# Performance work log

Measured on AMD Instinct MI355X. Metric: run time of the kernel, lower is better.

## Reference

```python
import jax, jax.numpy as jnp
import numpy as np

B, S, D = 4, 1024, 1280
H, DH = 20, 64          # n_head, d_hidden = embed_dim // n_head
DF = 4 * D              # r_ff = 4


def setup_inputs() -> dict:
    key = jax.random.key(0)
    ks = jax.random.split(key, 8)
    s_qkv = 1.0 / np.sqrt(D)
    inp = {
        "x": jax.random.normal(ks[0], (B, S, D), dtype=jnp.float32),
        # projection weights stored [in, out] so y = x @ W
        "Wq": jax.random.normal(ks[1], (D, H * DH), dtype=jnp.float32) * s_qkv,
        "Wk": jax.random.normal(ks[2], (D, H * DH), dtype=jnp.float32) * s_qkv,
        "Wv": jax.random.normal(ks[3], (D, H * DH), dtype=jnp.float32) * s_qkv,
        "ln_g": jnp.ones((D,), dtype=jnp.float32),
        "ln_b": jnp.zeros((D,), dtype=jnp.float32),
        "W1": jax.random.normal(ks[4], (D, DF), dtype=jnp.float32) * np.sqrt(2.0 / D),
        "b1": jnp.zeros((DF,), dtype=jnp.float32),
        "W2": jax.random.normal(ks[5], (DF, D), dtype=jnp.float32) * (1.0 / np.sqrt(DF)),
        "b2": jnp.zeros((D,), dtype=jnp.float32),
    }
    return inp


def reference(x, Wq, Wk, Wv, ln_g, ln_b, W1, b1, W2, b2):
    scaling = 1.0 / np.sqrt(DH)
    # --- Attention (note: original forward never applies to_out) ---
    q = (x @ Wq).reshape(B, S, H, DH) * scaling
    k = (x @ Wk).reshape(B, S, H, DH)
    v = (x @ Wv).reshape(B, S, H, DH)
    attn = jnp.einsum('bqhd,bkhd->bhqk', q, k)
    attn = jax.nn.softmax(attn, axis=-1)
    out = jnp.einsum('bhqk,bkhd->bqhd', attn, v).reshape(B, S, H * DH)
    x = out + x  # residual
    # --- FeedForward: LayerNorm -> linear1 -> relu -> linear2, residual ---
    mu = jnp.mean(x, axis=-1, keepdims=True)
    var = jnp.mean(jnp.square(x - mu), axis=-1, keepdims=True)
    h = (x - mu) * jax.lax.rsqrt(var + 1e-5) * ln_g + ln_b
    h = jax.nn.relu(h @ W1 + b1)
    h = h @ W2 + b2
    return x + h
```

## Files before the change

kernel.cpp:

```cpp
#include <hip/hip_runtime.h>
#include <hip/hip_bf16.h>

typedef short bf16x8 __attribute__((ext_vector_type(8)));
typedef float f32x4 __attribute__((ext_vector_type(4)));

typedef unsigned int u32_as1 __attribute__((address_space(1)));
typedef unsigned int u32_as3 __attribute__((address_space(3)));

#define B_ 4
#define S_ 1024
#define D_ 1280
#define H_ 20
#define DH_ 64
#define DF_ 5120
#define BS_ (B_*S_)
#define NQKV 3840

__device__ __forceinline__ void gld_lds16(const __hip_bfloat16* g, __hip_bfloat16* l) {
  __builtin_amdgcn_global_load_lds((const u32_as1*)g, (u32_as3*)l, 16, 0, 0);
}

__global__ __launch_bounds__(256) void cvt_f2b(
    const float* __restrict__ in, __hip_bfloat16* __restrict__ out, int n4)
{
  int i = blockIdx.x * 256 + threadIdx.x;
  if (i >= n4) return;
  const float4 v = ((const float4*)in)[i];
  __hip_bfloat16 o[4] = {__float2bfloat16(v.x), __float2bfloat16(v.y),
                         __float2bfloat16(v.z), __float2bfloat16(v.w)};
  *(short4*)(out + (size_t)i * 4) = *(short4*)o;
}

__global__ __launch_bounds__(256) void transpose_f2b(
    const float* __restrict__ in, __hip_bfloat16* __restrict__ out,
    int K, int N)
{
  __shared__ float tile[32][33];
  int k0 = blockIdx.x * 32, n0 = blockIdx.y * 32;
  int tx = threadIdx.x & 31, ty = threadIdx.x >> 5;
  #pragma unroll
  for (int i = 0; i < 32; i += 8)
    tile[ty + i][tx] = in[(size_t)(k0 + ty + i) * N + n0 + tx];
  __syncthreads();
  #pragma unroll
  for (int i = 0; i < 32; i += 8)
    out[(size_t)(n0 + ty + i) * K + k0 + tx] = __float2bfloat16(tile[tx][ty + i]);
}

__global__ __launch_bounds__(256) void transpose_v(
    const __hip_bfloat16* __restrict__ qkv, __hip_bfloat16* __restrict__ vT)
{
  __shared__ __hip_bfloat16 tile[32][33];
  int s0 = blockIdx.x * 32;
  int d0 = blockIdx.y * 32;
  int bh = blockIdx.z;
  int b = bh / H_, h = bh - b * H_;
  int tx = threadIdx.x & 31, ty = threadIdx.x >> 5;
  const __hip_bfloat16* src = qkv + (size_t)b * S_ * NQKV + 2 * D_ + h * DH_;
  #pragma unroll
  for (int i = 0; i < 32; i += 8)
    tile[ty + i][tx] = src[(size_t)(s0 + ty + i) * NQKV + d0 + tx];
  __syncthreads();
  __hip_bfloat16* dst = vT + (size_t)bh * DH_ * S_;
  #pragma unroll
  for (int i = 0; i < 32; i += 8)
    dst[(size_t)(d0 + ty + i) * S_ + s0 + tx] = tile[tx][ty + i];
}

template<int EPI>
__global__ __launch_bounds__(512, 2) void gemm256(
    const __hip_bfloat16* __restrict__ A,
    const __hip_bfloat16* __restrict__ BT,
    const float* __restrict__ bias,
    __hip_bfloat16* __restrict__ C,
    float* __restrict__ Cf0,
    float* __restrict__ Cf1,
    int M, int N, int K, int Kext)
{
  __shared__ __align__(16) __hip_bfloat16 As[2][2][256 * 32];
  __shared__ __align__(16) __hip_bfloat16 Bs[2][2][256 * 32];
  __hip_bfloat16* AsF = &As[0][0][0];
  __hip_bfloat16* BsF = &Bs[0][0][0];

  const int t = threadIdx.x;
  const int lane = t & 63;
  const int wave = t >> 6;
  const int wm = wave >> 2, wn = wave & 3;
  const int quad = lane >> 4, l16 = lane & 15;
  const int bm = blockIdx.x * 256, bn = blockIdx.y * 256;
  const int koff = blockIdx.z * Kext;
  const int Kc = (K - koff < Kext) ? (K - koff) : Kext;
  const int NT = Kc >> 6;

  const int srow = t >> 2;
  const int sc = (t & 3) ^ ((t >> 3) & 3);
  const __hip_bfloat16* Ag = A  + (size_t)(bm + srow) * K + koff + sc * 8;
  const __hip_bfloat16* Bg = BT + (size_t)(bn + srow) * K + koff + sc * 8;
  const size_t rq = (size_t)128 * K;

  const int swz = quad ^ ((l16 >> 1) & 3);
  const int aob = (wm * 128 + l16) * 32 + swz * 8;
  const int bob = (wn * 64 + l16) * 32 + swz * 8;

  f32x4 acc[8][4];
  #pragma unroll
  for (int i = 0; i < 8; i++)
    #pragma unroll
    for (int j = 0; j < 4; j++)
      acc[i][j] = (f32x4){0.f, 0.f, 0.f, 0.f};

#define STAGE_A(u_, kk_, b_) do { \
    const __hip_bfloat16* g_ = Ag + (size_t)(u_) * 64 + (kk_) * 32; \
    gld_lds16(g_,      AsF + ((b_) * 2 + (kk_)) * 8192 + t * 8); \
    gld_lds16(g_ + rq, AsF + ((b_) * 2 + (kk_)) * 8192 + 4096 + t * 8); \
  } while (0)
#define STAGE_B(u_, kk_, b_) do { \
    const __hip_bfloat16* g_ = Bg + (size_t)(u_) * 64 + (kk_) * 32; \
    gld_lds16(g_,      BsF + ((b_) * 2 + (kk_)) * 8192 + t * 8); \
    gld_lds16(g_ + rq, BsF + ((b_) * 2 + (kk_)) * 8192 + 4096 + t * 8); \
  } while (0)

  STAGE_A(0, 0, 0); STAGE_B(0, 0, 0); STAGE_A(0, 1, 0); STAGE_B(0, 1, 0);
  STAGE_B(1, 0, 1); STAGE_A(1, 0, 1); STAGE_B(1, 1, 1);
  asm volatile("s_waitcnt vmcnt(6)" ::: "memory");
  __builtin_amdgcn_s_barrier();
  asm volatile("" ::: "memory");

  bf16x8 av[4], bv[4];

#define PHASE_MFMA(ibase_) \
    __builtin_amdgcn_s_barrier(); \
    asm volatile("s_waitcnt lgkmcnt(0)" ::: "memory"); \
    __builtin_amdgcn_s_setprio(1); \
    _Pragma("unroll") \
    for (int i = 0; i < 4; i++) \
      _Pragma("unroll") \
      for (int j = 0; j < 4; j++) \
        acc[(ibase_) + i][j] = __builtin_amdgcn_mfma_f32_16x16x32_bf16(av[i], bv[j], acc[(ibase_) + i][j], 0, 0, 0); \
    __builtin_amdgcn_s_setprio(0); \
    __builtin_amdgcn_s_barrier(); \
    asm volatile("" ::: "memory");

#define TILE_BODY(u_, B_) do { \
    const int hb0 = (B_) * 2 * 8192, hb1 = ((B_) * 2 + 1) * 8192; \
     \
    _Pragma("unroll") \
    for (int i = 0; i < 4; i++) av[i] = *(const bf16x8*)(AsF + hb0 + aob + i * 512); \
    _Pragma("unroll") \
    for (int j = 0; j < 4; j++) bv[j] = *(const bf16x8*)(BsF + hb0 + bob + j * 512); \
    if ((u_) + 1 < NT) STAGE_A((u_) + 1, 1, (B_) ^ 1); \
    PHASE_MFMA(0) \
     \
    _Pragma("unroll") \
    for (int i = 0; i < 4; i++) av[i] = *(const bf16x8*)(AsF + hb0 + aob + (i + 4) * 512); \
    if ((u_) + 2 < NT) STAGE_B((u_) + 2, 0, (B_)); \
    PHASE_MFMA(4) \
     \
    _Pragma("unroll") \
    for (int i = 0; i < 4; i++) av[i] = *(const bf16x8*)(AsF + hb1 + aob + i * 512); \
    _Pragma("unroll") \
    for (int j = 0; j < 4; j++) bv[j] = *(const bf16x8*)(BsF + hb1 + bob + j * 512); \
    if ((u_) + 2 < NT) STAGE_A((u_) + 2, 0, (B_)); \
    PHASE_MFMA(0) \
     \
    _Pragma("unroll") \
    for (int i = 0; i < 4; i++) av[i] = *(const bf16x8*)(AsF + hb1 + aob + (i + 4) * 512); \
    if ((u_) + 2 < NT) { \
      STAGE_B((u_) + 2, 1, (B_)); \
      asm volatile("s_waitcnt vmcnt(6)" ::: "memory"); \
    } else { \
      asm volatile("s_waitcnt vmcnt(0)" ::: "memory"); \
    } \
    PHASE_MFMA(4) \
  } while (0)

  for (int u = 0; u < NT; u += 2) {
    TILE_BODY(u, 0);
    TILE_BODY(u + 1, 1);
  }

#undef TILE_BODY
#undef PHASE_MFMA
#undef STAGE_A
#undef STAGE_B

  float* Cf = (blockIdx.z == 0) ? Cf0 : Cf1;
  #pragma unroll
  for (int i = 0; i < 8; i++) {
    #pragma unroll
    for (int j = 0; j < 4; j++) {
      int col = bn + wn * 64 + j * 16 + l16;
      #pragma unroll
      for (int r = 0; r < 4; r++) {
        int row = bm + wm * 128 + i * 16 + quad * 4 + r;
        float v = acc[i][j][r];
        if (EPI == 1) { v += bias[col]; v = fmaxf(v, 0.f); }
        if (EPI == 3) {
          Cf[(size_t)row * N + col] = v;
        } else {
          C[(size_t)row * N + col] = __float2bfloat16(v);
        }
      }
    }
  }
}

__global__ __launch_bounds__(256) void ffn2_reduce(
    const float* __restrict__ P0, const float* __restrict__ P1,
    const float* __restrict__ bias, const float* __restrict__ resid,
    float* __restrict__ out)
{
  int i = blockIdx.x * 256 + threadIdx.x;
  float4 p0 = ((const float4*)P0)[i];
  float4 p1 = ((const float4*)P1)[i];
  float4 r  = ((const float4*)resid)[i];
  float4 b  = ((const float4*)bias)[i % (D_ / 4)];
  float4 o;
  o.x = p0.x + p1.x + r.x + b.x;
  o.y = p0.y + p1.y + r.y + b.y;
  o.z = p0.z + p1.z + r.z + b.z;
  o.w = p0.w + p1.w + r.w + b.w;
  ((float4*)out)[i] = o;
}

__global__ __launch_bounds__(256) void attn_mfma(
    const __hip_bfloat16* __restrict__ qkv,
    const __hip_bfloat16* __restrict__ vT,
    const float* __restrict__ x,
    float* __restrict__ x1)
{
  const int qt = blockIdx.x, h = blockIdx.y, b = blockIdx.z;
  const int t = threadIdx.x;
  const int lane = t & 63;
  const int wave = t >> 6;
  const int quad = lane >> 4, l16 = lane & 15;

  __shared__ __hip_bfloat16 Ks[2][64 * 64];
  __shared__ __hip_bfloat16 Vs[2][64 * 64];
  __shared__ short Pl[4][16][72];

  const int qrow0 = qt * 128 + wave * 32;
  const size_t tok0 = (size_t)b * S_;
  const int qcol = h * DH_;
  const int kcol = D_ + h * DH_;
  const size_t vtbase = (size_t)(b * H_ + h) * DH_ * S_;

  const int s1i = t + 256;
  const int r0 = t >> 3,   c0 = (t & 7)   ^ (r0 & 7);
  const int r1 = s1i >> 3, c1 = (s1i & 7) ^ (r1 & 7);
  const __hip_bfloat16* Kg0 = qkv + (tok0 + r0) * NQKV + kcol + c0 * 8;
  const __hip_bfloat16* Kg1 = qkv + (tok0 + r1) * NQKV + kcol + c1 * 8;
  const __hip_bfloat16* Vg0 = vT + vtbase + (size_t)r0 * S_ + c0 * 8;
  const __hip_bfloat16* Vg1 = vT + vtbase + (size_t)r1 * S_ + c1 * 8;
  const size_t kstep = (size_t)64 * NQKV;

  const float qscale = 0.125f * 1.44269504088896340736f;
  bf16x8 aq[2][2];
  #pragma unroll
  for (int m = 0; m < 2; m++)
    #pragma unroll
    for (int kc = 0; kc < 2; kc++) {
      bf16x8 raw = *(const bf16x8*)(qkv + (tok0 + qrow0 + m * 16 + l16) * NQKV
                                        + qcol + kc * 32 + quad * 8);
      bf16x8 scaled;
      #pragma unroll
      for (int j = 0; j < 8; j++) {
        float f = __uint_as_float(((unsigned)(unsigned short)raw[j]) << 16) * qscale;
        __hip_bfloat16 hb = __float2bfloat16(f);
        scaled[j] = *reinterpret_cast<short*>(&hb);
      }
      aq[m][kc] = scaled;
    }

  f32x4 O[2][4];
  float lsum[2][4];
  #pragma unroll
  for (int m = 0; m < 2; m++)
    #pragma unroll
    for (int n = 0; n < 4; n++) O[m][n] = (f32x4){0.f, 0.f, 0.f, 0.f};
  #pragma unroll
  for (int m = 0; m < 2; m++)
    #pragma unroll
    for (int r = 0; r < 4; r++) lsum[m][r] = 0.f;

  gld_lds16(Kg0, &Ks[0][t * 8]);
  gld_lds16(Kg1, &Ks[0][t * 8 + 2048]);
  gld_lds16(Vg0, &Vs[0][t * 8]);
  gld_lds16(Vg1, &Vs[0][t * 8 + 2048]);

  const int fsw = l16 & 7;

  for (int kt = 0; kt < S_ / 64; kt++) {
    const int buf = kt & 1;
    __syncthreads();

    if (kt + 1 < S_ / 64) {
      const int nb = buf ^ 1;
      gld_lds16(Kg0 + (size_t)(kt + 1) * kstep, &Ks[nb][t * 8]);
      gld_lds16(Kg1 + (size_t)(kt + 1) * kstep, &Ks[nb][t * 8 + 2048]);
      gld_lds16(Vg0 + (kt + 1) * 64, &Vs[nb][t * 8]);
      gld_lds16(Vg1 + (kt + 1) * 64, &Vs[nb][t * 8 + 2048]);
    }

    bf16x8 kb[4][2];
    #pragma unroll
    for (int j = 0; j < 4; j++)
      #pragma unroll
      for (int kc = 0; kc < 2; kc++)
        kb[j][kc] = *(const bf16x8*)&Ks[buf][(j * 16 + l16) * 64
                                            + (((kc * 4 + quad) ^ fsw) * 8)];
    f32x4 sc[2][4];
    #pragma unroll
    for (int m = 0; m < 2; m++)
      #pragma unroll
      for (int j = 0; j < 4; j++) {
        sc[m][j] = (f32x4){0.f, 0.f, 0.f, 0.f};
        sc[m][j] = __builtin_amdgcn_mfma_f32_16x16x32_bf16(aq[m][0], kb[j][0], sc[m][j], 0, 0, 0);
        sc[m][j] = __builtin_amdgcn_mfma_f32_16x16x32_bf16(aq[m][1], kb[j][1], sc[m][j], 0, 0, 0);
      }

    bf16x8 vb[4][2];
    #pragma unroll
    for (int n = 0; n < 4; n++)
      #pragma unroll
      for (int kc = 0; kc < 2; kc++)
        vb[n][kc] = *(const bf16x8*)&Vs[buf][(n * 16 + l16) * 64
                                            + (((kc * 4 + quad) ^ fsw) * 8)];

    #pragma unroll
    for (int m = 0; m < 2; m++) {
      #pragma unroll
      for (int j = 0; j < 4; j++)
        #pragma unroll
        for (int r = 0; r < 4; r++) {
          float p = exp2f(sc[m][j][r]);
          lsum[m][r] += p;
          Pl[wave][quad * 4 + r][j * 16 + l16] = (short)(__float_as_uint(p) >> 16);
        }
      bf16x8 pa0 = *(const bf16x8*)&Pl[wave][l16][quad * 8];
      bf16x8 pa1 = *(const bf16x8*)&Pl[wave][l16][32 + quad * 8];
      #pragma unroll
      for (int n = 0; n < 4; n++) {
        O[m][n] = __builtin_amdgcn_mfma_f32_16x16x32_bf16(pa0, vb[n][0], O[m][n], 0, 0, 0);
        O[m][n] = __builtin_amdgcn_mfma_f32_16x16x32_bf16(pa1, vb[n][1], O[m][n], 0, 0, 0);
      }
    }
  }

  #pragma unroll
  for (int m = 0; m < 2; m++)
    #pragma unroll
    for (int r = 0; r < 4; r++) {
      float s = lsum[m][r];
      s += __shfl_xor(s, 1);
      s += __shfl_xor(s, 2);
      s += __shfl_xor(s, 4);
      s += __shfl_xor(s, 8);
      lsum[m][r] = 1.f / s;
    }

  #pragma unroll
  for (int m = 0; m < 2; m++)
    #pragma unroll
    for (int n = 0; n < 4; n++)
      #pragma unroll
      for (int r = 0; r < 4; r++) {
        size_t row = tok0 + qrow0 + m * 16 + quad * 4 + r;
        int col = qcol + n * 16 + l16;
        size_t idx = row * D_ + col;
        x1[idx] = O[m][n][r] * lsum[m][r] + x[idx];
      }
}

__global__ __launch_bounds__(256) void ln_kernel(
    const float* __restrict__ x1, const float* __restrict__ g,
    const float* __restrict__ bta, __hip_bfloat16* __restrict__ h)
{
  int row = blockIdx.x, t = threadIdx.x;
  __shared__ float red[256];
  float v[5];
  size_t base = (size_t)row * D_;
  #pragma unroll
  for (int i = 0; i < 5; i++) v[i] = x1[base + t + 256 * i];
  float s = v[0] + v[1] + v[2] + v[3] + v[4];
  red[t] = s; __syncthreads();
  for (int off = 128; off; off >>= 1) {
    if (t < off) red[t] += red[t + off];
    __syncthreads();
  }
  float mu = red[0] * (1.f / D_);
  __syncthreads();
  float sq = 0.f;
  #pragma unroll
  for (int i = 0; i < 5; i++) { float d = v[i] - mu; sq += d * d; }
  red[t] = sq; __syncthreads();
  for (int off = 128; off; off >>= 1) {
    if (t < off) red[t] += red[t + off];
    __syncthreads();
  }
  float rs = rsqrtf(red[0] * (1.f / D_) + 1e-5f);
  #pragma unroll
  for (int i = 0; i < 5; i++) {
    int c = t + 256 * i;
    float hv = (v[i] - mu) * rs * g[c] + bta[c];
    h[base + c] = __float2bfloat16(hv);
  }
}

extern "C" void kernel_launch(void* const* d_in, const int* in_sizes, int n_in,
                              void* d_out, int out_size, void* d_ws, size_t ws_size,
                              hipStream_t stream) {
  (void)in_sizes; (void)n_in; (void)out_size; (void)ws_size;
  const float* x   = (const float*)d_in[0];
  const float* Wq  = (const float*)d_in[1];
  const float* Wk  = (const float*)d_in[2];
  const float* Wv  = (const float*)d_in[3];
  const float* lng = (const float*)d_in[4];
  const float* lnb = (const float*)d_in[5];
  const float* W1  = (const float*)d_in[6];
  const float* b1  = (const float*)d_in[7];
  const float* W2  = (const float*)d_in[8];
  const float* b2  = (const float*)d_in[9];
  float* out = (float*)d_out;

  char* ws = (char*)d_ws;
  size_t o = 0;
  __hip_bfloat16* W2T = (__hip_bfloat16*)(ws + o); o += (size_t)D_ * DF_ * 2;
  float*          x1  = (float*)(ws + o);          o += (size_t)BS_ * D_ * 4;
  char* regA = ws + o; o += (size_t)DF_ * D_ * 2 + (size_t)BS_ * D_ * 2;
  __hip_bfloat16* W1T  = (__hip_bfloat16*)regA;
  __hip_bfloat16* hbuf = (__hip_bfloat16*)(regA + (size_t)DF_ * D_ * 2);
  float*          P0   = (float*)regA;
  char* regB = ws + o;
  __hip_bfloat16* xb    = (__hip_bfloat16*)regB;
  __hip_bfloat16* BTqkv = (__hip_bfloat16*)(regB + (size_t)BS_ * D_ * 2);
  __hip_bfloat16* qkv   = (__hip_bfloat16*)(regB + (size_t)BS_ * D_ * 2
                                                 + (size_t)NQKV * D_ * 2);
  __hip_bfloat16* vT    = (__hip_bfloat16*)(regB + (size_t)BS_ * D_ * 2
                                                 + (size_t)NQKV * D_ * 2
                                                 + (size_t)BS_ * NQKV * 2);
  float*          P1    = (float*)regB;
  __hip_bfloat16* gbuf  = (__hip_bfloat16*)(regB + (size_t)BS_ * D_ * 4);

  transpose_f2b<<<dim3(D_/32, D_/32), 256, 0, stream>>>(Wq, BTqkv,                   D_, D_);
  transpose_f2b<<<dim3(D_/32, D_/32), 256, 0, stream>>>(Wk, BTqkv + (size_t)D_*D_,   D_, D_);
  transpose_f2b<<<dim3(D_/32, D_/32), 256, 0, stream>>>(Wv, BTqkv + (size_t)2*D_*D_, D_, D_);
  transpose_f2b<<<dim3(D_/32, DF_/32), 256, 0, stream>>>(W1, W1T, D_, DF_);
  transpose_f2b<<<dim3(DF_/32, D_/32), 256, 0, stream>>>(W2, W2T, DF_, D_);
  cvt_f2b<<<(BS_*D_/4 + 255)/256, 256, 0, stream>>>(x, xb, BS_*D_/4);

  gemm256<0><<<dim3(BS_/256, NQKV/256), 512, 0, stream>>>(
      xb, BTqkv, nullptr, qkv, nullptr, nullptr, BS_, NQKV, D_, D_);
  transpose_v<<<dim3(S_/32, DH_/32, B_*H_), 256, 0, stream>>>(qkv, vT);
  attn_mfma<<<dim3(S_/128, H_, B_), 256, 0, stream>>>(qkv, vT, x, x1);
  ln_kernel<<<BS_, 256, 0, stream>>>(x1, lng, lnb, hbuf);
  gemm256<1><<<dim3(BS_/256, DF_/256), 512, 0, stream>>>(
      hbuf, W1T, b1, gbuf, nullptr, nullptr, BS_, DF_, D_, D_);
  gemm256<3><<<dim3(BS_/256, D_/256, 2), 512, 0, stream>>>(
      gbuf, W2T, nullptr, nullptr, P0, P1, BS_, D_, DF_, DF_/2);
  ffn2_reduce<<<BS_*D_/4/256, 256, 0, stream>>>(P0, P1, b2, x1, out);
}
```

Measured before the change: 426.7 us.

## Add 256x128 GEMM kernel for FFN layers and move vmcnt wait after MFMAs

Adds a gemm128 kernel with 256x128 output tiles, 8 waves each owning 64x64, and launch bounds allowing two blocks per CU. The two FFN GEMMs now use it, doubling the number of blocks to fill more of the CUs on a 304-CU part, because the 256x256 grid gave few blocks (e.g. 80 for FFN2 with split-K). The gemm256 tail also moves the vmcnt wait after the MFMA phase so global loads overlap compute. In exchange, the smaller tile lowers arithmetic intensity and adds more B traffic.

```diff
diff --git a/kernel.cpp b/kernel.cpp
--- a/kernel.cpp
+++ b/kernel.cpp
@@ -141,6 +141,21 @@
     __builtin_amdgcn_s_barrier(); \
     asm volatile("" ::: "memory");
 
+#define PHASE_MFMA_TAIL(ibase_, last_) \
+    __builtin_amdgcn_s_barrier(); \
+    asm volatile("s_waitcnt lgkmcnt(0)" ::: "memory"); \
+    __builtin_amdgcn_s_setprio(1); \
+    _Pragma("unroll") \
+    for (int i = 0; i < 4; i++) \
+      _Pragma("unroll") \
+      for (int j = 0; j < 4; j++) \
+        acc[(ibase_) + i][j] = __builtin_amdgcn_mfma_f32_16x16x32_bf16(av[i], bv[j], acc[(ibase_) + i][j], 0, 0, 0); \
+    __builtin_amdgcn_s_setprio(0); \
+    if (last_) { asm volatile("s_waitcnt vmcnt(0)" ::: "memory"); } \
+    else       { asm volatile("s_waitcnt vmcnt(6)" ::: "memory"); } \
+    __builtin_amdgcn_s_barrier(); \
+    asm volatile("" ::: "memory");
+
 #define TILE_BODY(u_, B_) do { \
     const int hb0 = (B_) * 2 * 8192, hb1 = ((B_) * 2 + 1) * 8192; \
      \
@@ -165,13 +180,8 @@
      \
     _Pragma("unroll") \
     for (int i = 0; i < 4; i++) av[i] = *(const bf16x8*)(AsF + hb1 + aob + (i + 4) * 512); \
-    if ((u_) + 2 < NT) { \
-      STAGE_B((u_) + 2, 1, (B_)); \
-      asm volatile("s_waitcnt vmcnt(6)" ::: "memory"); \
-    } else { \
-      asm volatile("s_waitcnt vmcnt(0)" ::: "memory"); \
-    } \
-    PHASE_MFMA(4) \
+    if ((u_) + 2 < NT) STAGE_B((u_) + 2, 1, (B_)); \
+    PHASE_MFMA_TAIL(4, (u_) + 2 >= NT) \
   } while (0)
 
   for (int u = 0; u < NT; u += 2) {
@@ -181,6 +191,7 @@
 
 #undef TILE_BODY
 #undef PHASE_MFMA
+#undef PHASE_MFMA_TAIL
 #undef STAGE_A
 #undef STAGE_B
 
@@ -193,6 +204,133 @@
       #pragma unroll
       for (int r = 0; r < 4; r++) {
         int row = bm + wm * 128 + i * 16 + quad * 4 + r;
+        float v = acc[i][j][r];
+        if (EPI == 1) { v += bias[col]; v = fmaxf(v, 0.f); }
+        if (EPI == 3) {
+          Cf[(size_t)row * N + col] = v;
+        } else {
+          C[(size_t)row * N + col] = __float2bfloat16(v);
+        }
+      }
+    }
+  }
+}
+
+template<int EPI>
+__global__ __launch_bounds__(512, 2) void gemm128(
+    const __hip_bfloat16* __restrict__ A,
+    const __hip_bfloat16* __restrict__ BT,
+    const float* __restrict__ bias,
+    __hip_bfloat16* __restrict__ C,
+    float* __restrict__ Cf0,
+    float* __restrict__ Cf1,
+    int M, int N, int K, int Kext)
+{
+  __shared__ __align__(16) __hip_bfloat16 As[2][2][256 * 32];
+  __shared__ __align__(16) __hip_bfloat16 Bs[2][2][128 * 32];
+  __hip_bfloat16* AsF = &As[0][0][0];
+  __hip_bfloat16* BsF = &Bs[0][0][0];
+
+  const int t = threadIdx.x;
+  const int lane = t & 63;
+  const int wave = t >> 6;
+  const int wm = wave >> 1, wn = wave & 1;
+  const int quad = lane >> 4, l16 = lane & 15;
+  const int bm = blockIdx.x * 256, bn = blockIdx.y * 128;
+  const int koff = blockIdx.z * Kext;
+  const int Kc = (K - koff < Kext) ? (K - koff) : Kext;
+  const int NT = Kc >> 6;
+
+  const int srow = t >> 2;
+  const int sc = (t & 3) ^ ((t >> 3) & 3);
+  const __hip_bfloat16* Ag = A  + (size_t)(bm + srow) * K + koff + sc * 8;
+  const __hip_bfloat16* Bg = BT + (size_t)(bn + srow) * K + koff + sc * 8;
+  const size_t rq = (size_t)128 * K;
+
+  const int swz = quad ^ ((l16 >> 1) & 3);
+  const int aob = (wm * 64 + l16) * 32 + swz * 8;
+  const int bob = (wn * 64 + l16) * 32 + swz * 8;
+
+  f32x4 acc[4][4];
+  #pragma unroll
+  for (int i = 0; i < 4; i++)
+    #pragma unroll
+    for (int j = 0; j < 4; j++)
+      acc[i][j] = (f32x4){0.f, 0.f, 0.f, 0.f};
+
+#define STAGE_A1(u_, kk_, b_) do { \
+    const __hip_bfloat16* g_ = Ag + (size_t)(u_) * 64 + (kk_) * 32; \
+    gld_lds16(g_,      AsF + ((b_) * 2 + (kk_)) * 8192 + t * 8); \
+    gld_lds16(g_ + rq, AsF + ((b_) * 2 + (kk_)) * 8192 + 4096 + t * 8); \
+  } while (0)
+#define STAGE_B1(u_, kk_, b_) do { \
+    const __hip_bfloat16* g_ = Bg + (size_t)(u_) * 64 + (kk_) * 32; \
+    gld_lds16(g_, BsF + ((b_) * 2 + (kk_)) * 4096 + t * 8); \
+  } while (0)
+
+  STAGE_A1(0, 0, 0); STAGE_B1(0, 0, 0); STAGE_A1(0, 1, 0); STAGE_B1(0, 1, 0);
+  STAGE_A1(1, 0, 1); STAGE_B1(1, 0, 1);
+  asm volatile("s_waitcnt vmcnt(3)" ::: "memory");
+  __builtin_amdgcn_s_barrier();
+  asm volatile("" ::: "memory");
+
+  bf16x8 av[4], bv[4];
+
+#define PHASE128(tail_, last_) \
+    __builtin_amdgcn_s_barrier(); \
+    asm volatile("s_waitcnt lgkmcnt(0)" ::: "memory"); \
+    __builtin_amdgcn_s_setprio(1); \
+    _Pragma("unroll") \
+    for (int i = 0; i < 4; i++) \
+      _Pragma("unroll") \
+      for (int j = 0; j < 4; j++) \
+        acc[i][j] = __builtin_amdgcn_mfma_f32_16x16x32_bf16(av[i], bv[j], acc[i][j], 0, 0, 0); \
+    __builtin_amdgcn_s_setprio(0); \
+    if (tail_) { \
+      if (last_) { asm volatile("s_waitcnt vmcnt(0)" ::: "memory"); } \
+      else       { asm volatile("s_waitcnt vmcnt(3)" ::: "memory"); } \
+    } \
+    __builtin_amdgcn_s_barrier(); \
+    asm volatile("" ::: "memory");
+
+#define TILE128(u_, B_) do { \
+    const int ha0 = (B_) * 2 * 8192, ha1 = ((B_) * 2 + 1) * 8192; \
+    const int hbb0 = (B_) * 2 * 4096, hbb1 = ((B_) * 2 + 1) * 4096; \
+     \
+    _Pragma("unroll") \
+    for (int i = 0; i < 4; i++) av[i] = *(const bf16x8*)(AsF + ha0 + aob + i * 512); \
+    _Pragma("unroll") \
+    for (int j = 0; j < 4; j++) bv[j] = *(const bf16x8*)(BsF + hbb0 + bob + j * 512); \
+    if ((u_) + 1 < NT) { STAGE_A1((u_) + 1, 1, (B_) ^ 1); STAGE_B1((u_) + 1, 1, (B_) ^ 1); } \
+    PHASE128(0, 0) \
+     \
+    _Pragma("unroll") \
+    for (int i = 0; i < 4; i++) av[i] = *(const bf16x8*)(AsF + ha1 + aob + i * 512); \
+    _Pragma("unroll") \
+    for (int j = 0; j < 4; j++) bv[j] = *(const bf16x8*)(BsF + hbb1 + bob + j * 512); \
+    if ((u_) + 2 < NT) { STAGE_A1((u_) + 2, 0, (B_)); STAGE_B1((u_) + 2, 0, (B_)); } \
+    PHASE128(1, (u_) + 2 >= NT) \
+  } while (0)
+
+  for (int u = 0; u < NT; u += 2) {
+    TILE128(u, 0);
+    TILE128(u + 1, 1);
+  }
+
+#undef TILE128
+#undef PHASE128
+#undef STAGE_A1
+#undef STAGE_B1
+
+  float* Cf = (blockIdx.z == 0) ? Cf0 : Cf1;
+  #pragma unroll
+  for (int i = 0; i < 4; i++) {
+    #pragma unroll
+    for (int j = 0; j < 4; j++) {
+      int col = bn + wn * 64 + j * 16 + l16;
+      #pragma unroll
+      for (int r = 0; r < 4; r++) {
+        int row = bm + wm * 64 + i * 16 + quad * 4 + r;
         float v = acc[i][j][r];
         if (EPI == 1) { v += bias[col]; v = fmaxf(v, 0.f); }
         if (EPI == 3) {
@@ -454,9 +592,9 @@
   transpose_v<<<dim3(S_/32, DH_/32, B_*H_), 256, 0, stream>>>(qkv, vT);
   attn_mfma<<<dim3(S_/128, H_, B_), 256, 0, stream>>>(qkv, vT, x, x1);
   ln_kernel<<<BS_, 256, 0, stream>>>(x1, lng, lnb, hbuf);
-  gemm256<1><<<dim3(BS_/256, DF_/256), 512, 0, stream>>>(
+  gemm128<1><<<dim3(BS_/256, DF_/128), 512, 0, stream>>>(
       hbuf, W1T, b1, gbuf, nullptr, nullptr, BS_, DF_, D_, D_);
-  gemm256<3><<<dim3(BS_/256, D_/256, 2), 512, 0, stream>>>(
+  gemm128<3><<<dim3(BS_/256, D_/128, 2), 512, 0, stream>>>(
       gbuf, W2T, nullptr, nullptr, P0, P1, BS_, D_, DF_, DF_/2);
   ffn2_reduce<<<BS_*D_/4/256, 256, 0, stream>>>(P0, P1, b2, x1, out);
 }
```

Measured after the change: 448.9 us. 1.05x slower.

## Split FFN2 GEMM K three ways and swizzle workgroup order across XCDs

Applied to the files above, without the earlier changes.

The second FFN GEMM now splits K into three uneven chunks instead of two, which raises the grid from 80 to 120 workgroups to fill more CUs. The third partial is written into the output buffer and summed by the reduce kernel. The GEMM also remaps workgroup IDs so that consecutive tiles land on the same XCD, aiming for better L2 reuse. The cost is an extra fp32 partial to write and read back, and the uneven K chunks (1792 and 1664) must stay multiples of 128 for the two-tile loop to be correct.

```diff
diff --git a/kernel.cpp b/kernel.cpp
--- a/kernel.cpp
+++ b/kernel.cpp
@@ -75,7 +75,8 @@
     __hip_bfloat16* __restrict__ C,
     float* __restrict__ Cf0,
     float* __restrict__ Cf1,
-    int M, int N, int K, int Kext)
+    float* __restrict__ Cf2,
+    int M, int N, int K, int KextA, int KextR)
 {
   __shared__ __align__(16) __hip_bfloat16 As[2][2][256 * 32];
   __shared__ __align__(16) __hip_bfloat16 Bs[2][2][256 * 32];
@@ -87,9 +88,21 @@
   const int wave = t >> 6;
   const int wm = wave >> 2, wn = wave & 3;
   const int quad = lane >> 4, l16 = lane & 15;
-  const int bm = blockIdx.x * 256, bn = blockIdx.y * 256;
-  const int koff = blockIdx.z * Kext;
-  const int Kc = (K - koff < Kext) ? (K - koff) : Kext;
+
+  const int gx = gridDim.x;
+  const int nwg = gx * gridDim.y;
+  int orig = blockIdx.y * gx + blockIdx.x;
+  int bx = blockIdx.x, by = blockIdx.y;
+  if ((nwg & 7) == 0) {
+    const int q = nwg >> 3;
+    const int swz = (orig & 7) * q + (orig >> 3);
+    bx = swz % gx; by = swz / gx;
+  }
+  const int bm = bx * 256, bn = by * 256;
+
+  const int z = blockIdx.z;
+  const int koff = (z == 0) ? 0 : (KextA + (z - 1) * KextR);
+  const int Kc = (z == 0) ? KextA : KextR;
   const int NT = Kc >> 6;
 
   const int srow = t >> 2;
@@ -98,9 +111,9 @@
   const __hip_bfloat16* Bg = BT + (size_t)(bn + srow) * K + koff + sc * 8;
   const size_t rq = (size_t)128 * K;
 
-  const int swz = quad ^ ((l16 >> 1) & 3);
-  const int aob = (wm * 128 + l16) * 32 + swz * 8;
-  const int bob = (wn * 64 + l16) * 32 + swz * 8;
+  const int swzf = quad ^ ((l16 >> 1) & 3);
+  const int aob = (wm * 128 + l16) * 32 + swzf * 8;
+  const int bob = (wn * 64 + l16) * 32 + swzf * 8;
 
   f32x4 acc[8][4];
   #pragma unroll
@@ -184,7 +197,7 @@
 #undef STAGE_A
 #undef STAGE_B
 
-  float* Cf = (blockIdx.z == 0) ? Cf0 : Cf1;
+  float* Cf = (z == 0) ? Cf0 : ((z == 1) ? Cf1 : Cf2);
   #pragma unroll
   for (int i = 0; i < 8; i++) {
     #pragma unroll
@@ -205,7 +218,7 @@
   }
 }
 
-__global__ __launch_bounds__(256) void ffn2_reduce(
+__global__ __launch_bounds__(256) void ffn2_reduce3(
     const float* __restrict__ P0, const float* __restrict__ P1,
     const float* __restrict__ bias, const float* __restrict__ resid,
     float* __restrict__ out)
@@ -213,13 +226,14 @@
   int i = blockIdx.x * 256 + threadIdx.x;
   float4 p0 = ((const float4*)P0)[i];
   float4 p1 = ((const float4*)P1)[i];
+  float4 p2 = ((const float4*)out)[i];
   float4 r  = ((const float4*)resid)[i];
   float4 b  = ((const float4*)bias)[i % (D_ / 4)];
   float4 o;
-  o.x = p0.x + p1.x + r.x + b.x;
-  o.y = p0.y + p1.y + r.y + b.y;
-  o.z = p0.z + p1.z + r.z + b.z;
-  o.w = p0.w + p1.w + r.w + b.w;
+  o.x = p0.x + p1.x + p2.x + r.x + b.x;
+  o.y = p0.y + p1.y + p2.y + r.y + b.y;
+  o.z = p0.z + p1.z + p2.z + r.z + b.z;
+  o.w = p0.w + p1.w + p2.w + r.w + b.w;
   ((float4*)out)[i] = o;
 }
 
@@ -441,6 +455,7 @@
                                                  + (size_t)BS_ * NQKV * 2);
   float*          P1    = (float*)regB;
   __hip_bfloat16* gbuf  = (__hip_bfloat16*)(regB + (size_t)BS_ * D_ * 4);
+  float*          P2    = out;
 
   transpose_f2b<<<dim3(D_/32, D_/32), 256, 0, stream>>>(Wq, BTqkv,                   D_, D_);
   transpose_f2b<<<dim3(D_/32, D_/32), 256, 0, stream>>>(Wk, BTqkv + (size_t)D_*D_,   D_, D_);
@@ -450,13 +465,13 @@
   cvt_f2b<<<(BS_*D_/4 + 255)/256, 256, 0, stream>>>(x, xb, BS_*D_/4);
 
   gemm256<0><<<dim3(BS_/256, NQKV/256), 512, 0, stream>>>(
-      xb, BTqkv, nullptr, qkv, nullptr, nullptr, BS_, NQKV, D_, D_);
+      xb, BTqkv, nullptr, qkv, nullptr, nullptr, nullptr, BS_, NQKV, D_, D_, D_);
   transpose_v<<<dim3(S_/32, DH_/32, B_*H_), 256, 0, stream>>>(qkv, vT);
   attn_mfma<<<dim3(S_/128, H_, B_), 256, 0, stream>>>(qkv, vT, x, x1);
   ln_kernel<<<BS_, 256, 0, stream>>>(x1, lng, lnb, hbuf);
   gemm256<1><<<dim3(BS_/256, DF_/256), 512, 0, stream>>>(
-      hbuf, W1T, b1, gbuf, nullptr, nullptr, BS_, DF_, D_, D_);
-  gemm256<3><<<dim3(BS_/256, D_/256, 2), 512, 0, stream>>>(
-      gbuf, W2T, nullptr, nullptr, P0, P1, BS_, D_, DF_, DF_/2);
-  ffn2_reduce<<<BS_*D_/4/256, 256, 0, stream>>>(P0, P1, b2, x1, out);
-}
+      hbuf, W1T, b1, gbuf, nullptr, nullptr, nullptr, BS_, DF_, D_, D_, D_);
+  gemm256<3><<<dim3(BS_/256, D_/256, 3), 512, 0, stream>>>(
+      gbuf, W2T, nullptr, nullptr, P0, P1, P2, BS_, D_, DF_, 1792, 1664);
+  ffn2_reduce3<<<BS_*D_/4/256, 256, 0, stream>>>(P0, P1, b2, x1, out);
+}
```

New measurement: 410.4 us. 1.04x faster.
